# Kernel tuning notes

Hardware: AMD Instinct MI355X
Metric: run time of the kernel (lower is better)

Reference implementation:

```python
import jax, jax.numpy as jnp
import numpy as np

BS, N = 8, 2000
ALPHA = 0.2  # LeakyReLU slope
NEG = -9e15


def _gat_head(x, adj, W, a):
    # x: [bs,N,Fin], W: [Fin,Fout], a: [2*Fout]
    h = x @ W                                   # [bs,N,F]
    F_ = W.shape[-1]
    # e_ij = lrelu(h_i . a[:F] + h_j . a[F:])  (decomposed form of concat+matmul)
    src = h @ a[:F_]                            # [bs,N]
    dst = h @ a[F_:]                            # [bs,N]
    e = jax.nn.leaky_relu(src[:, :, None] + dst[:, None, :], ALPHA)  # [bs,N,N]
    att = jnp.where(adj[None] > 0, e, NEG)
    att = jax.nn.softmax(att, axis=-1)
    return jax.nn.elu(att @ h)                  # [bs,N,F]


def _gat_multihead(x, adj, W, a):
    # W: [H,Fin,Fout], a: [H,2*Fout] -> concat heads on feature dim
    out = jax.vmap(_gat_head, in_axes=(None, None, 0, 0))(x, adj, W, a)  # [H,bs,N,F]
    H, bs, n, F_ = out.shape
    return jnp.moveaxis(out, 0, 2).reshape(bs, n, H * F_)


def setup_inputs() -> dict:
    key = jax.random.key(0)
    ks = jax.random.split(key, 20)
    g = 1.414

    def xavu(k, shape, gain=1.0):
        fan_in, fan_out = shape[-2], shape[-1]
        lim = gain * np.sqrt(6.0 / (fan_in + fan_out))
        return jax.random.uniform(k, shape, jnp.float32, -lim, lim)

    x = jax.random.normal(ks[0], (BS, N, 1), jnp.float32)
    adj = jax.random.randint(ks[1], (N, N), 0, 2).astype(jnp.float32)
    inp = {
        "x": x, "adj": adj,
        "W1": xavu(ks[2], (4, 1, 8), g), "a1": xavu(ks[3], (4, 16, 1), g)[..., 0],
        "W2": xavu(ks[4], (3, 32, 16), g), "a2": xavu(ks[5], (3, 32, 1), g)[..., 0],
        "pw1": xavu(ks[6], (32, 1))[:, 0], "pb1": jnp.zeros((1,), jnp.float32),
        "pw2": xavu(ks[7], (48, 1))[:, 0], "pb2": jnp.zeros((1,), jnp.float32),
        "fc1_w": xavu(ks[8], (3 * N, 600)), "fc1_b": jnp.zeros((600,), jnp.float32),
        "fc2_w": xavu(ks[9], (600, 256)), "fc2_b": jnp.zeros((256,), jnp.float32),
        "fc3_w": xavu(ks[10], (256, 64)), "fc3_b": jnp.zeros((64,), jnp.float32),
        "fc4_w": xavu(ks[11], (64, 32)), "fc4_b": jnp.zeros((32,), jnp.float32),
        "fc5_w": xavu(ks[12], (32, 2)), "fc5_b": jnp.zeros((2,), jnp.float32),
    }
    return inp


def reference(x, adj, W1, a1, W2, a2, pw1, pb1, pw2, pb2,
              fc1_w, fc1_b, fc2_w, fc2_b, fc3_w, fc3_b, fc4_w, fc4_b, fc5_w, fc5_b):
    # dropout layers are identity in eval mode
    x0 = jnp.mean(x, axis=-1)                       # [bs,N]
    h = _gat_multihead(x, adj, W1, a1)              # [bs,N,32]
    x1 = h @ pw1 + pb1                              # [bs,N]
    h = _gat_multihead(h, adj, W2, a2)              # [bs,N,48]
    x2 = h @ pw2 + pb2                              # [bs,N]
    z = jnp.concatenate([x0, x1, x2], axis=1)       # [bs,3N]
    z = jax.nn.elu(z @ fc1_w + fc1_b)
    z = jax.nn.elu(z @ fc2_w + fc2_b)
    z1 = jax.nn.elu(z @ fc3_w + fc3_b)              # output [bs,64]
    z = jax.nn.elu(z1 @ fc4_w + fc4_b)
    gat_out = z @ fc5_w + fc5_b                     # [bs,2]
    return (z1, gat_out)
```

## Files before the change

### kernel.cpp

```cpp
#include <hip/hip_runtime.h>
#include <hip/hip_bf16.h>
#include <cmath>

#define N_NODES 2000
#define BS 8

typedef __attribute__((ext_vector_type(8))) short short8v;
typedef __attribute__((ext_vector_type(4))) float float4v;

__device__ __forceinline__ float elu_f(float v) { return v > 0.f ? v : expm1f(v); }

__device__ __forceinline__ short f32_bf16(float f) {
    __hip_bfloat16 h = __float2bfloat16(f);
    unsigned short u;
    __builtin_memcpy(&u, &h, 2);
    return (short)u;
}

__device__ __forceinline__ float sel_mask(float w, unsigned long long m) {
    float r;
    asm("v_cndmask_b32 %0, 0, %1, %2" : "=v"(r) : "v"(w), "s"(m));
    return r;
}

__global__ __launch_bounds__(256) void pack_kernel(
    const float* __restrict__ adj, const float* __restrict__ x,
    const float* __restrict__ W1, const float* __restrict__ a1,
    unsigned long long* __restrict__ maskT, unsigned* __restrict__ maskT32,
    float* __restrict__ s1, float* __restrict__ d1,
    short* __restrict__ hT) {
    int bx = blockIdx.x;
    int tid = threadIdx.x;
    if (bx < N_NODES) {
        int row = bx;
        int lane = tid & 63, wv = tid >> 6;
        for (int wq = wv; wq < 32; wq += 4) {
            int j = wq * 64 + lane;
            bool on = (j < N_NODES) && (adj[(size_t)row * N_NODES + j] > 0.f);
            unsigned long long bal = __ballot(on);
            if (lane == 0) {
                maskT[(size_t)wq * 2048 + row] = bal;
                maskT32[(size_t)(2 * wq) * 2048 + row] = (unsigned)bal;
                maskT32[(size_t)(2 * wq + 1) * 2048 + row] = (unsigned)(bal >> 32);
            }
        }
        return;
    }
    if (bx < N_NODES + 32) {
        int bh = bx - N_NODES;
        int b = bh >> 2, h = bh & 3;
        float ws = 0.f, wd = 0.f;
        #pragma unroll
        for (int f = 0; f < 8; ++f) {
            float wv = W1[h * 8 + f];
            ws = fmaf(wv, a1[h * 16 + f], ws);
            wd = fmaf(wv, a1[h * 16 + 8 + f], wd);
        }
        for (int n = tid; n < N_NODES; n += 256) {
            float xv = x[b * N_NODES + n];
            s1[(size_t)bh * N_NODES + n] = xv * ws;
            d1[(size_t)bh * N_NODES + n] = xv * wd;
        }
        return;
    }
    for (int i = tid; i < 24 * 16 * 48; i += 256) {
        int bh = i / 768, rem = i % 768, f = rem / 48, n = N_NODES + rem % 48;
        hT[((size_t)bh * 16 + f) * 2048 + n] = 0;
    }
}

__global__ __launch_bounds__(256) void att1_kernel(
    const unsigned long long* __restrict__ maskT,
    const float* __restrict__ x,
    const float* __restrict__ s1, const float* __restrict__ d1,
    const float* __restrict__ W1,
    float* __restrict__ o1) {
    __shared__ float2 sPQ[2048];
    __shared__ float red[256];
    int tid = threadIdx.x;
    int head = blockIdx.y, b = blockIdx.z, bh = b * 4 + head;
    const float* dp = d1 + (size_t)bh * N_NODES;

    float mx = -1e30f;
    for (int n = tid; n < N_NODES; n += 256) mx = fmaxf(mx, dp[n]);
    red[tid] = mx;
    __syncthreads();
    for (int s = 128; s > 0; s >>= 1) {
        if (tid < s) red[tid] = fmaxf(red[tid], red[tid + s]);
        __syncthreads();
    }
    float md = red[0];
    for (int n = tid; n < 2048; n += 256) {
        if (n < N_NODES) {
            float d = dp[n] - md;
            sPQ[n] = make_float2(__expf(d), __expf(0.2f * d));
        } else {
            sPQ[n] = make_float2(0.f, 0.f);
        }
    }
    __syncthreads();

    int lane = tid & 63;
    int wave = __builtin_amdgcn_readfirstlane(tid >> 6);
    int t = blockIdx.x * 4 + wave;
    if (t >= 250) return;
    int row0 = t * 8;

    float Ar[8], Br[8], num[8], den[8];
    #pragma unroll
    for (int r = 0; r < 8; ++r) {
        float sv = s1[(size_t)bh * N_NODES + row0 + r];
        float u = sv + md, ub = fmaxf(u, 0.2f * u);
        Ar[r] = __expf(u - ub);
        Br[r] = __expf(0.2f * u - ub);
        num[r] = 0.f; den[r] = 0.f;
    }

    for (int j0 = 0; j0 < 2048; j0 += 64) {
        int j = j0 + lane;
        float2 pq = sPQ[j];
        float xv = (j < N_NODES) ? x[(size_t)b * N_NODES + j] : 0.f;
        const unsigned long long* mrow = maskT + ((size_t)(j0 >> 6) << 11) + row0;
        #pragma unroll
        for (int r = 0; r < 8; ++r) {
            float w = fmaxf(Ar[r] * pq.x, Br[r] * pq.y);
            w = sel_mask(w, mrow[r]);
            num[r] = fmaf(w, xv, num[r]);
            den[r] += w;
        }
    }
    #pragma unroll
    for (int off = 32; off >= 1; off >>= 1) {
        #pragma unroll
        for (int r = 0; r < 8; ++r) {
            num[r] += __shfl_xor(num[r], off, 64);
            den[r] += __shfl_xor(den[r], off, 64);
        }
    }
    if (lane < 8) {
        float wf = W1[head * 8 + lane];
        #pragma unroll
        for (int r = 0; r < 8; ++r) {
            float ratio = den[r] > 0.f ? num[r] / den[r] : 0.f;
            float v = ratio * wf;
            o1[((size_t)(b * N_NODES + row0 + r)) * 32 + head * 8 + lane] =
                v > 0.f ? v : expm1f(v);
        }
    }
}

__global__ __launch_bounds__(256) void prep2_kernel(
    const float* __restrict__ o1, const float* __restrict__ W2,
    const float* __restrict__ a2,
    short* __restrict__ hT, float* __restrict__ s2, float* __restrict__ d2) {
    __shared__ float sW[1536];
    int tid = threadIdx.x;
    for (int i = tid; i < 1536; i += 256) sW[i] = W2[i];
    __syncthreads();
    int idx = blockIdx.x * 256 + tid;
    if (idx >= BS * 3 * N_NODES) return;
    int b = idx / 6000, r = idx % 6000, h = r / N_NODES, n = r % N_NODES;
    int bh = b * 3 + h;
    float in[32];
    const float4* ip = (const float4*)(o1 + ((size_t)b * N_NODES + n) * 32);
    #pragma unroll
    for (int q = 0; q < 8; ++q) {
        float4 v = ip[q];
        in[4 * q] = v.x; in[4 * q + 1] = v.y; in[4 * q + 2] = v.z; in[4 * q + 3] = v.w;
    }
    float hv[16];
    #pragma unroll
    for (int f = 0; f < 16; ++f) hv[f] = 0.f;
    #pragma unroll
    for (int k = 0; k < 32; ++k) {
        float ik = in[k];
        #pragma unroll
        for (int f = 0; f < 16; ++f) hv[f] = fmaf(ik, sW[h * 512 + k * 16 + f], hv[f]);
    }
    float sr = 0.f, ds = 0.f;
    #pragma unroll
    for (int f = 0; f < 16; ++f) {
        hT[((size_t)bh * 16 + f) * 2048 + n] = f32_bf16(hv[f]);
        sr = fmaf(hv[f], a2[h * 32 + f], sr);
        ds = fmaf(hv[f], a2[h * 32 + 16 + f], ds);
    }
    s2[(size_t)bh * N_NODES + n] = sr;
    d2[(size_t)bh * N_NODES + n] = ds;
}

__global__ __launch_bounds__(256) void att2_kernel(
    const unsigned* __restrict__ maskT32,
    const short* __restrict__ hT,
    const float* __restrict__ s2, const float* __restrict__ d2,
    float* __restrict__ o2) {
    __shared__ float2 sPQ[2048];
    __shared__ float red[256];
    int tid = threadIdx.x;
    int head = blockIdx.y, b = blockIdx.z, bh = b * 3 + head;
    const float* dp = d2 + (size_t)bh * N_NODES;

    float mx = -1e30f;
    for (int n = tid; n < N_NODES; n += 256) mx = fmaxf(mx, dp[n]);
    red[tid] = mx;
    __syncthreads();
    for (int s = 128; s > 0; s >>= 1) {
        if (tid < s) red[tid] = fmaxf(red[tid], red[tid + s]);
        __syncthreads();
    }
    float md = red[0];
    for (int n = tid; n < 2048; n += 256) {
        if (n < N_NODES) {
            float d = dp[n] - md;
            sPQ[n] = make_float2(__expf(d), __expf(0.2f * d));
        } else {
            sPQ[n] = make_float2(0.f, 0.f);
        }
    }
    __syncthreads();

    int lane = tid & 63;
    int wave = __builtin_amdgcn_readfirstlane(tid >> 6);
    int t = blockIdx.x * 4 + wave;
    if (t >= 125) return;
    int rs = lane & 15;
    int g = lane >> 4;
    int row = t * 16 + rs;

    float sv = s2[(size_t)bh * N_NODES + row];
    float u = sv + md, ub = fmaxf(u, 0.2f * u);
    float Ar = __expf(u - ub), Br = __expf(0.2f * u - ub);
    const short* hb = hT + ((size_t)bh * 16 + rs) * 2048;

    float4v acc = {0.f, 0.f, 0.f, 0.f};
    float den = 0.f;

    for (int jc = 0; jc < 64; ++jc) {
        int jb = jc * 32 + g * 8;
        float w[8];
        #pragma unroll
        for (int e2 = 0; e2 < 4; ++e2) {
            float4 pq2 = *(const float4*)(&sPQ[jb + e2 * 2]);
            w[e2 * 2 + 0] = fmaxf(Ar * pq2.x, Br * pq2.y);
            w[e2 * 2 + 1] = fmaxf(Ar * pq2.z, Br * pq2.w);
        }
        unsigned mby = maskT32[(size_t)jc * 2048 + row] >> (g * 8);
        short8v av;
        #pragma unroll
        for (int e = 0; e < 8; ++e) {
            float we = (mby & (1u << e)) ? w[e] : 0.f;
            den += we;
            av[e] = f32_bf16(we);
        }
        short8v bv = *(const short8v*)(hb + jb);
        acc = __builtin_amdgcn_mfma_f32_16x16x32_bf16(av, bv, acc, 0, 0, 0);
    }

    den += __shfl_xor(den, 16, 64);
    den += __shfl_xor(den, 32, 64);
    float inv = den > 0.f ? 1.0f / den : 0.f;

    #pragma unroll
    for (int reg = 0; reg < 4; ++reg) {
        int crow = g * 4 + reg;
        float invr = __shfl(inv, crow, 64);
        float v = acc[reg] * invr;
        v = v > 0.f ? v : expm1f(v);
        o2[((size_t)(b * N_NODES + t * 16 + crow)) * 48 + head * 16 + rs] = v;
    }
}

__global__ __launch_bounds__(256) void fc1_splitk_kernel(
    const float* __restrict__ x,
    const float* __restrict__ o1, const float* __restrict__ o2,
    const float* __restrict__ pw1, const float* __restrict__ pb1,
    const float* __restrict__ pw2, const float* __restrict__ pb2,
    const float* __restrict__ W, float* __restrict__ partial) {
    const int K = 6000, O = 600, KS = 71;
    __shared__ float sz[BS][KS];
    int tid = threadIdx.x;
    int kt = blockIdx.y;
    int k0 = kt * KS;
    int len = (k0 + KS <= K) ? KS : (K - k0);
    float pb1v = pb1[0], pb2v = pb2[0];
    for (int i = tid; i < BS * len; i += 256) {
        int bb = i / len, k = k0 + i % len;
        float v;
        if (k < 2000) {
            v = x[bb * 2000 + k];
        } else if (k < 4000) {
            const float* op = o1 + ((size_t)bb * 2000 + (k - 2000)) * 32;
            float s = pb1v;
            #pragma unroll
            for (int q = 0; q < 32; ++q) s = fmaf(op[q], pw1[q], s);
            v = s;
        } else {
            const float* op = o2 + ((size_t)bb * 2000 + (k - 4000)) * 48;
            float s = pb2v;
            #pragma unroll
            for (int q = 0; q < 48; ++q) s = fmaf(op[q], pw2[q], s);
            v = s;
        }
        sz[bb][i % len] = v;
    }
    __syncthreads();
    int o = blockIdx.x * 256 + tid;
    float acc[BS] = {0.f, 0.f, 0.f, 0.f, 0.f, 0.f, 0.f, 0.f};
    if (o < O) {
        for (int k = 0; k < len; ++k) {
            float w = W[(size_t)(k0 + k) * O + o];
            #pragma unroll
            for (int b = 0; b < BS; ++b) acc[b] = fmaf(sz[b][k], w, acc[b]);
        }
        #pragma unroll
        for (int b = 0; b < BS; ++b)
            partial[((size_t)kt * BS + b) * O + o] = acc[b];
    }
}

__global__ __launch_bounds__(256) void fc_reduce1_kernel(
    const float* __restrict__ p1, const float* __restrict__ bias,
    float* __restrict__ t1) {
    int o = blockIdx.x * 256 + threadIdx.x;
    int b = blockIdx.y;
    if (o >= 600) return;
    float a = bias[o];
    #pragma unroll 5
    for (int kt = 0; kt < 85; ++kt) a += p1[((size_t)kt * BS + b) * 600 + o];
    t1[(size_t)b * 600 + o] = elu_f(a);
}

__global__ __launch_bounds__(256) void fc2_splitk_kernel(
    const float* __restrict__ in, const float* __restrict__ W,
    float* __restrict__ partial) {
    const int K = 600, O = 256, KS = 38;
    __shared__ float sz[BS][KS];
    int tid = threadIdx.x;
    int kt = blockIdx.y;
    int k0 = kt * KS;
    int k1 = k0 + KS < K ? k0 + KS : K;
    int len = k1 - k0;
    for (int i = tid; i < BS * len; i += 256)
        sz[i / len][i % len] = in[(size_t)(i / len) * K + k0 + i % len];
    __syncthreads();
    int o = tid;
    float acc[BS] = {0.f, 0.f, 0.f, 0.f, 0.f, 0.f, 0.f, 0.f};
    for (int k = 0; k < len; ++k) {
        float w = W[(size_t)(k0 + k) * O + o];
        #pragma unroll
        for (int b = 0; b < BS; ++b) acc[b] = fmaf(sz[b][k], w, acc[b]);
    }
    #pragma unroll
    for (int b = 0; b < BS; ++b)
        partial[((size_t)kt * BS + b) * O + o] = acc[b];
}

__global__ __launch_bounds__(256) void fc_tail_kernel(
    const float* __restrict__ p2, const float* __restrict__ b2,
    const float* __restrict__ w3, const float* __restrict__ b3,
    const float* __restrict__ w4, const float* __restrict__ b4,
    const float* __restrict__ w5, const float* __restrict__ b5,
    float* __restrict__ outp) {
    int b = blockIdx.x, tid = threadIdx.x;
    __shared__ float t2[256], red[256], z1[64], z4[32];
    {
        float a = b2[tid];
        #pragma unroll
        for (int kt = 0; kt < 16; ++kt) a += p2[((size_t)kt * BS + b) * 256 + tid];
        t2[tid] = elu_f(a);
    }
    __syncthreads();
    {
        int o = tid & 63, ks = tid >> 6;
        float a = 0.f;
        for (int k = ks; k < 256; k += 4) a = fmaf(t2[k], w3[k * 64 + o], a);
        red[tid] = a;
        __syncthreads();
        if (ks == 0) {
            float v = red[o] + red[64 + o] + red[128 + o] + red[192 + o] + b3[o];
            v = elu_f(v);
            z1[o] = v;
            outp[b * 64 + o] = v;
        }
    }
    __syncthreads();
    if (tid < 32) {
        float v = b4[tid];
        #pragma unroll
        for (int k = 0; k < 64; ++k) v = fmaf(z1[k], w4[k * 32 + tid], v);
        z4[tid] = elu_f(v);
    }
    __syncthreads();
    if (tid < 2) {
        float v = b5[tid];
        #pragma unroll
        for (int k = 0; k < 32; ++k) v = fmaf(z4[k], w5[k * 2 + tid], v);
        outp[BS * 64 + b * 2 + tid] = v;
    }
}

extern "C" void kernel_launch(void* const* d_in, const int* in_sizes, int n_in,
                              void* d_out, int out_size, void* d_ws, size_t ws_size,
                              hipStream_t stream) {
    const float* x    = (const float*)d_in[0];
    const float* adj  = (const float*)d_in[1];
    const float* W1   = (const float*)d_in[2];
    const float* a1   = (const float*)d_in[3];
    const float* W2   = (const float*)d_in[4];
    const float* a2   = (const float*)d_in[5];
    const float* pw1  = (const float*)d_in[6];
    const float* pb1  = (const float*)d_in[7];
    const float* pw2  = (const float*)d_in[8];
    const float* pb2  = (const float*)d_in[9];
    const float* fc1w = (const float*)d_in[10];
    const float* fc1b = (const float*)d_in[11];
    const float* fc2w = (const float*)d_in[12];
    const float* fc2b = (const float*)d_in[13];
    const float* fc3w = (const float*)d_in[14];
    const float* fc3b = (const float*)d_in[15];
    const float* fc4w = (const float*)d_in[16];
    const float* fc4b = (const float*)d_in[17];
    const float* fc5w = (const float*)d_in[18];
    const float* fc5b = (const float*)d_in[19];
    float* outp = (float*)d_out;

    float* ws = (float*)d_ws;
    size_t off = 0;
    auto alloc = [&](size_t n) {
        float* p = ws + off;
        off += (n + 63) & ~(size_t)63;
        return p;
    };
    float* s1 = alloc((size_t)32 * N_NODES);
    float* d1 = alloc((size_t)32 * N_NODES);
    float* o1 = alloc((size_t)BS * N_NODES * 32);
    float* s2 = alloc((size_t)24 * N_NODES);
    float* d2 = alloc((size_t)24 * N_NODES);
    short* hT = (short*)alloc((size_t)24 * 16 * 2048 / 2);
    float* o2 = alloc((size_t)BS * N_NODES * 48);
    const int KT1 = 85;
    float* p1 = alloc((size_t)KT1 * BS * 600);
    float* t1 = alloc((size_t)BS * 600);
    float* p2 = alloc((size_t)16 * BS * 256);
    unsigned long long* maskT = (unsigned long long*)alloc((size_t)32 * 2048 * 2);
    unsigned* maskT32 = (unsigned*)alloc((size_t)64 * 2048);

    pack_kernel<<<N_NODES + 32 + 1, 256, 0, stream>>>(
        adj, x, W1, a1, maskT, maskT32, s1, d1, hT);
    att1_kernel<<<dim3(63, 4, BS), 256, 0, stream>>>(maskT, x, s1, d1, W1, o1);
    prep2_kernel<<<(BS * 3 * N_NODES + 255) / 256, 256, 0, stream>>>(o1, W2, a2, hT, s2, d2);
    att2_kernel<<<dim3(32, 3, BS), 256, 0, stream>>>(maskT32, hT, s2, d2, o2);
    fc1_splitk_kernel<<<dim3(3, KT1), 256, 0, stream>>>(
        x, o1, o2, pw1, pb1, pw2, pb2, fc1w, p1);
    fc_reduce1_kernel<<<dim3(3, BS), 256, 0, stream>>>(p1, fc1b, t1);
    fc2_splitk_kernel<<<dim3(1, 16), 256, 0, stream>>>(t1, fc2w, p2);
    fc_tail_kernel<<<BS, 256, 0, stream>>>(
        p2, fc2b, fc3w, fc3b, fc4w, fc4b, fc5w, fc5b, outp);
}
```

Baseline: 130.1 us.

## Fuse layer-1 score computation into attention kernel, process two heads per block

Removes the separate s1/d1 precompute from the pack kernel. att1 now derives source/destination scores on the fly from x and the folded W1·a1 vectors, taking the max from the min/max of x. Each att1 block now handles two heads, sharing the mask loads and staged x values, and stores the P/Q exponentials as packed bf16 in LDS to halve the table size. The fc1 reduction kernel is folded into fc2_splitk, which redoes the 85-way partial sum per block. These changes drop one launch and several global round-trips, but add redundant reduction work in fc2, bf16 rounding of the attention weights, and a larger per-thread register footprint.

```diff
diff --git a/kernel.cpp b/kernel.cpp
--- a/kernel.cpp
+++ b/kernel.cpp
@@ -10,12 +10,13 @@
 
 __device__ __forceinline__ float elu_f(float v) { return v > 0.f ? v : expm1f(v); }
 
-__device__ __forceinline__ short f32_bf16(float f) {
+__device__ __forceinline__ unsigned short f32_bf16u(float f) {
     __hip_bfloat16 h = __float2bfloat16(f);
     unsigned short u;
     __builtin_memcpy(&u, &h, 2);
-    return (short)u;
-}
+    return u;
+}
+__device__ __forceinline__ short f32_bf16(float f) { return (short)f32_bf16u(f); }
 
 __device__ __forceinline__ float sel_mask(float w, unsigned long long m) {
     float r;
@@ -24,10 +25,8 @@
 }
 
 __global__ __launch_bounds__(256) void pack_kernel(
-    const float* __restrict__ adj, const float* __restrict__ x,
-    const float* __restrict__ W1, const float* __restrict__ a1,
+    const float* __restrict__ adj,
     unsigned long long* __restrict__ maskT, unsigned* __restrict__ maskT32,
-    float* __restrict__ s1, float* __restrict__ d1,
     short* __restrict__ hT) {
     int bx = blockIdx.x;
     int tid = threadIdx.x;
@@ -46,23 +45,6 @@
         }
         return;
     }
-    if (bx < N_NODES + 32) {
-        int bh = bx - N_NODES;
-        int b = bh >> 2, h = bh & 3;
-        float ws = 0.f, wd = 0.f;
-        #pragma unroll
-        for (int f = 0; f < 8; ++f) {
-            float wv = W1[h * 8 + f];
-            ws = fmaf(wv, a1[h * 16 + f], ws);
-            wd = fmaf(wv, a1[h * 16 + 8 + f], wd);
-        }
-        for (int n = tid; n < N_NODES; n += 256) {
-            float xv = x[b * N_NODES + n];
-            s1[(size_t)bh * N_NODES + n] = xv * ws;
-            d1[(size_t)bh * N_NODES + n] = xv * wd;
-        }
-        return;
-    }
     for (int i = tid; i < 24 * 16 * 48; i += 256) {
         int bh = i / 768, rem = i % 768, f = rem / 48, n = N_NODES + rem % 48;
         hT[((size_t)bh * 16 + f) * 2048 + n] = 0;
@@ -72,30 +54,58 @@
 __global__ __launch_bounds__(256) void att1_kernel(
     const unsigned long long* __restrict__ maskT,
     const float* __restrict__ x,
-    const float* __restrict__ s1, const float* __restrict__ d1,
-    const float* __restrict__ W1,
+    const float* __restrict__ W1, const float* __restrict__ a1,
     float* __restrict__ o1) {
-    __shared__ float2 sPQ[2048];
-    __shared__ float red[256];
-    int tid = threadIdx.x;
-    int head = blockIdx.y, b = blockIdx.z, bh = b * 4 + head;
-    const float* dp = d1 + (size_t)bh * N_NODES;
-
-    float mx = -1e30f;
-    for (int n = tid; n < N_NODES; n += 256) mx = fmaxf(mx, dp[n]);
-    red[tid] = mx;
+    __shared__ unsigned sPQ[2][2048];
+    __shared__ float sX[2048];
+    __shared__ float2 redmm[256];
+    int tid = threadIdx.x;
+    int by = blockIdx.y, b = blockIdx.z;
+
+    float mn = 1e30f, mx = -1e30f;
+    for (int n = tid; n < 2048; n += 256) {
+        float xv = (n < N_NODES) ? x[(size_t)b * N_NODES + n] : 0.f;
+        sX[n] = xv;
+        if (n < N_NODES) { mn = fminf(mn, xv); mx = fmaxf(mx, xv); }
+    }
+    redmm[tid] = make_float2(mn, mx);
     __syncthreads();
     for (int s = 128; s > 0; s >>= 1) {
-        if (tid < s) red[tid] = fmaxf(red[tid], red[tid + s]);
+        if (tid < s) {
+            redmm[tid].x = fminf(redmm[tid].x, redmm[tid + s].x);
+            redmm[tid].y = fmaxf(redmm[tid].y, redmm[tid + s].y);
+        }
         __syncthreads();
     }
-    float md = red[0];
+    float xmin = redmm[0].x, xmax = redmm[0].y;
+
+    float wsv[2], wdv[2], md[2];
+    #pragma unroll
+    for (int hh = 0; hh < 2; ++hh) {
+        int head = by * 2 + hh;
+        float ws = 0.f, wd = 0.f;
+        #pragma unroll
+        for (int f = 0; f < 8; ++f) {
+            float wv = W1[head * 8 + f];
+            ws = fmaf(wv, a1[head * 16 + f], ws);
+            wd = fmaf(wv, a1[head * 16 + 8 + f], wd);
+        }
+        wsv[hh] = ws; wdv[hh] = wd;
+        md[hh] = wd >= 0.f ? wd * xmax : wd * xmin;
+    }
+
     for (int n = tid; n < 2048; n += 256) {
-        if (n < N_NODES) {
-            float d = dp[n] - md;
-            sPQ[n] = make_float2(__expf(d), __expf(0.2f * d));
-        } else {
-            sPQ[n] = make_float2(0.f, 0.f);
+        float xv = sX[n];
+        #pragma unroll
+        for (int hh = 0; hh < 2; ++hh) {
+            unsigned v = 0;
+            if (n < N_NODES) {
+                float d = wdv[hh] * xv - md[hh];
+                unsigned Pb = f32_bf16u(__expf(d));
+                unsigned Qb = f32_bf16u(__expf(0.2f * d));
+                v = (Pb << 16) | Qb;
+            }
+            sPQ[hh][n] = v;
         }
     }
     __syncthreads();
@@ -106,45 +116,65 @@
     if (t >= 250) return;
     int row0 = t * 8;
 
-    float Ar[8], Br[8], num[8], den[8];
-    #pragma unroll
-    for (int r = 0; r < 8; ++r) {
-        float sv = s1[(size_t)bh * N_NODES + row0 + r];
-        float u = sv + md, ub = fmaxf(u, 0.2f * u);
-        Ar[r] = __expf(u - ub);
-        Br[r] = __expf(0.2f * u - ub);
-        num[r] = 0.f; den[r] = 0.f;
+    float A_[2][8], B_[2][8], num[2][8], den[2][8];
+    #pragma unroll
+    for (int hh = 0; hh < 2; ++hh) {
+        #pragma unroll
+        for (int r = 0; r < 8; ++r) {
+            float sv = wsv[hh] * sX[row0 + r];
+            float u = sv + md[hh], ub = fmaxf(u, 0.2f * u);
+            A_[hh][r] = __expf(u - ub);
+            B_[hh][r] = __expf(0.2f * u - ub);
+            num[hh][r] = 0.f; den[hh][r] = 0.f;
+        }
     }
 
     for (int j0 = 0; j0 < 2048; j0 += 64) {
         int j = j0 + lane;
-        float2 pq = sPQ[j];
-        float xv = (j < N_NODES) ? x[(size_t)b * N_NODES + j] : 0.f;
+        unsigned pq0 = sPQ[0][j];
+        unsigned pq1 = sPQ[1][j];
+        float xv = sX[j];
+        float P0 = __uint_as_float(pq0 & 0xFFFF0000u);
+        float Q0 = __uint_as_float(pq0 << 16);
+        float P1 = __uint_as_float(pq1 & 0xFFFF0000u);
+        float Q1 = __uint_as_float(pq1 << 16);
         const unsigned long long* mrow = maskT + ((size_t)(j0 >> 6) << 11) + row0;
         #pragma unroll
         for (int r = 0; r < 8; ++r) {
-            float w = fmaxf(Ar[r] * pq.x, Br[r] * pq.y);
-            w = sel_mask(w, mrow[r]);
-            num[r] = fmaf(w, xv, num[r]);
-            den[r] += w;
+            unsigned long long m = mrow[r];
+            float w0 = fmaxf(A_[0][r] * P0, B_[0][r] * Q0);
+            w0 = sel_mask(w0, m);
+            num[0][r] = fmaf(w0, xv, num[0][r]);
+            den[0][r] += w0;
+            float w1 = fmaxf(A_[1][r] * P1, B_[1][r] * Q1);
+            w1 = sel_mask(w1, m);
+            num[1][r] = fmaf(w1, xv, num[1][r]);
+            den[1][r] += w1;
         }
     }
     #pragma unroll
     for (int off = 32; off >= 1; off >>= 1) {
         #pragma unroll
-        for (int r = 0; r < 8; ++r) {
-            num[r] += __shfl_xor(num[r], off, 64);
-            den[r] += __shfl_xor(den[r], off, 64);
+        for (int hh = 0; hh < 2; ++hh) {
+            #pragma unroll
+            for (int r = 0; r < 8; ++r) {
+                num[hh][r] += __shfl_xor(num[hh][r], off, 64);
+                den[hh][r] += __shfl_xor(den[hh][r], off, 64);
+            }
         }
     }
     if (lane < 8) {
-        float wf = W1[head * 8 + lane];
-        #pragma unroll
-        for (int r = 0; r < 8; ++r) {
-            float ratio = den[r] > 0.f ? num[r] / den[r] : 0.f;
-            float v = ratio * wf;
-            o1[((size_t)(b * N_NODES + row0 + r)) * 32 + head * 8 + lane] =
-                v > 0.f ? v : expm1f(v);
+        #pragma unroll
+        for (int hh = 0; hh < 2; ++hh) {
+            int head = by * 2 + hh;
+            float wf = W1[head * 8 + lane];
+            #pragma unroll
+            for (int r = 0; r < 8; ++r) {
+                float ratio = den[hh][r] > 0.f ? num[hh][r] / den[hh][r] : 0.f;
+                float v = ratio * wf;
+                o1[((size_t)(b * N_NODES + row0 + r)) * 32 + head * 8 + lane] =
+                    v > 0.f ? v : expm1f(v);
+            }
         }
     }
 }
@@ -317,21 +347,9 @@
     }
 }
 
-__global__ __launch_bounds__(256) void fc_reduce1_kernel(
-    const float* __restrict__ p1, const float* __restrict__ bias,
-    float* __restrict__ t1) {
-    int o = blockIdx.x * 256 + threadIdx.x;
-    int b = blockIdx.y;
-    if (o >= 600) return;
-    float a = bias[o];
-    #pragma unroll 5
-    for (int kt = 0; kt < 85; ++kt) a += p1[((size_t)kt * BS + b) * 600 + o];
-    t1[(size_t)b * 600 + o] = elu_f(a);
-}
-
 __global__ __launch_bounds__(256) void fc2_splitk_kernel(
-    const float* __restrict__ in, const float* __restrict__ W,
-    float* __restrict__ partial) {
+    const float* __restrict__ p1, const float* __restrict__ b1,
+    const float* __restrict__ W, float* __restrict__ partial) {
     const int K = 600, O = 256, KS = 38;
     __shared__ float sz[BS][KS];
     int tid = threadIdx.x;
@@ -339,8 +357,13 @@
     int k0 = kt * KS;
     int k1 = k0 + KS < K ? k0 + KS : K;
     int len = k1 - k0;
-    for (int i = tid; i < BS * len; i += 256)
-        sz[i / len][i % len] = in[(size_t)(i / len) * K + k0 + i % len];
+    for (int i = tid; i < BS * len; i += 256) {
+        int bb = i / len, k = k0 + i % len;
+        float a = b1[k];
+        #pragma unroll 5
+        for (int q = 0; q < 85; ++q) a += p1[((size_t)q * BS + bb) * 600 + k];
+        sz[bb][i % len] = elu_f(a);
+    }
     __syncthreads();
     int o = tid;
     float acc[BS] = {0.f, 0.f, 0.f, 0.f, 0.f, 0.f, 0.f, 0.f};
@@ -430,8 +453,6 @@
         off += (n + 63) & ~(size_t)63;
         return p;
     };
-    float* s1 = alloc((size_t)32 * N_NODES);
-    float* d1 = alloc((size_t)32 * N_NODES);
     float* o1 = alloc((size_t)BS * N_NODES * 32);
     float* s2 = alloc((size_t)24 * N_NODES);
     float* d2 = alloc((size_t)24 * N_NODES);
@@ -439,20 +460,17 @@
     float* o2 = alloc((size_t)BS * N_NODES * 48);
     const int KT1 = 85;
     float* p1 = alloc((size_t)KT1 * BS * 600);
-    float* t1 = alloc((size_t)BS * 600);
     float* p2 = alloc((size_t)16 * BS * 256);
     unsigned long long* maskT = (unsigned long long*)alloc((size_t)32 * 2048 * 2);
     unsigned* maskT32 = (unsigned*)alloc((size_t)64 * 2048);
 
-    pack_kernel<<<N_NODES + 32 + 1, 256, 0, stream>>>(
-        adj, x, W1, a1, maskT, maskT32, s1, d1, hT);
-    att1_kernel<<<dim3(63, 4, BS), 256, 0, stream>>>(maskT, x, s1, d1, W1, o1);
+    pack_kernel<<<N_NODES + 1, 256, 0, stream>>>(adj, maskT, maskT32, hT);
+    att1_kernel<<<dim3(63, 2, BS), 256, 0, stream>>>(maskT, x, W1, a1, o1);
     prep2_kernel<<<(BS * 3 * N_NODES + 255) / 256, 256, 0, stream>>>(o1, W2, a2, hT, s2, d2);
     att2_kernel<<<dim3(32, 3, BS), 256, 0, stream>>>(maskT32, hT, s2, d2, o2);
     fc1_splitk_kernel<<<dim3(3, KT1), 256, 0, stream>>>(
         x, o1, o2, pw1, pb1, pw2, pb2, fc1w, p1);
-    fc_reduce1_kernel<<<dim3(3, BS), 256, 0, stream>>>(p1, fc1b, t1);
-    fc2_splitk_kernel<<<dim3(1, 16), 256, 0, stream>>>(t1, fc2w, p2);
+    fc2_splitk_kernel<<<dim3(1, 16), 256, 0, stream>>>(p1, fc1b, fc2w, p2);
     fc_tail_kernel<<<BS, 256, 0, stream>>>(
         p2, fc2b, fc3w, fc3b, fc4w, fc4b, fc5w, fc5b, outp);
 }
```

Result: slower. 136.1 us (+4.6%).
